# Kernel optimization log

Measured on AMD Instinct MI355X. Metric: run time of the kernel, lower is better.

The kernel has to match this reference:

```python
import jax, jax.numpy as jnp
import numpy as np

B, T_SRC, T_TGT = 32, 64, 64
V_KO, V_EN, E, H = 32000, 32000, 512, 512  # decoder hidden = 2H


def _lstm_step(x, h, c, Wih, Whh, b):
    # PyTorch gate order: i, f, g, o
    g = x @ Wih.T + h @ Whh.T + b
    i, f, gg, o = jnp.split(g, 4, axis=-1)
    c = jax.nn.sigmoid(f) * c + jax.nn.sigmoid(i) * jnp.tanh(gg)
    h = jax.nn.sigmoid(o) * jnp.tanh(c)
    return h, c


def _run_lstm(emb, Wih, Whh, b, hdim):
    # emb: [T, B, E] -> outputs [T, B, hdim], last (h, c)
    nb = emb.shape[1]
    init = (jnp.zeros((nb, hdim), emb.dtype), jnp.zeros((nb, hdim), emb.dtype))
    def step(carry, x):
        h, c = _lstm_step(x, carry[0], carry[1], Wih, Whh, b)
        return (h, c), h
    (h, c), outs = jax.lax.scan(step, init, emb)
    return outs, h, c


def setup_inputs() -> dict:
    key = jax.random.key(0)
    ks = jax.random.split(key, 16)
    s = 0.05
    d = {
        "inp": jax.random.randint(ks[0], (B, T_SRC), 0, V_KO),
        "tar": jax.random.randint(ks[1], (B, T_TGT), 0, V_EN),
        "enc_emb": jax.random.normal(ks[2], (V_KO, E)) * s,
        "dec_emb": jax.random.normal(ks[3], (V_EN, E)) * s,
        # BiLSTM encoder (forward / backward directions)
        "Wih_f": jax.random.normal(ks[4], (4 * H, E)) * s,
        "Whh_f": jax.random.normal(ks[5], (4 * H, H)) * s,
        "b_f": jnp.zeros((4 * H,)),
        "Wih_b": jax.random.normal(ks[6], (4 * H, E)) * s,
        "Whh_b": jax.random.normal(ks[7], (4 * H, H)) * s,
        "b_b": jnp.zeros((4 * H,)),
        # Concat (Bahdanau) attention: W [2H, 4H], v [2H]
        "Wa": jax.random.normal(ks[8], (2 * H, 4 * H)) * s,
        "va": jax.random.normal(ks[9], (2 * H,)) * s,
        # Decoder LSTMCell: input E + 2H, hidden 2H
        "Wih_d": jax.random.normal(ks[10], (8 * H, E + 2 * H)) * s,
        "Whh_d": jax.random.normal(ks[11], (8 * H, 2 * H)) * s,
        "b_d": jnp.zeros((8 * H,)),
        # Output projection
        "Wout": jax.random.normal(ks[12], (V_EN, 2 * H)) * s,
        "bout": jnp.zeros((V_EN,)),
    }
    return d


def reference(inp, tar, enc_emb, dec_emb, Wih_f, Whh_f, b_f, Wih_b, Whh_b, b_b,
              Wa, va, Wih_d, Whh_d, b_d, Wout, bout):
    # ---- Encoder: BiLSTM over source ----
    emb = enc_emb[inp].transpose(1, 0, 2)  # [T_src, B, E]
    out_f, hf, cf = _run_lstm(emb, Wih_f, Whh_f, b_f, H)
    out_b, hb, cb = _run_lstm(emb[::-1], Wih_b, Whh_b, b_b, H)
    enc_out = jnp.concatenate([out_f, out_b[::-1]], axis=-1)  # [T_src, B, 2H]
    h = jnp.concatenate([hf, hb], axis=-1)  # [B, 2H]
    c = jnp.concatenate([cf, cb], axis=-1)

    # ---- Decoder: teacher forcing with concat attention ----
    dec_e = dec_emb[tar].transpose(1, 0, 2)  # [T_tgt, B, E]
    Tsrc = enc_out.shape[0]

    def step(carry, x):
        h, c = carry
        hq = jnp.broadcast_to(h[None], (Tsrc,) + h.shape)         # [T_src, B, 2H]
        energy = jnp.tanh(jnp.concatenate([hq, enc_out], -1) @ Wa.T)  # [T_src, B, 2H]
        score = energy @ va                                        # [T_src, B]
        alpha = jax.nn.softmax(score, axis=0)
        cvec = jnp.einsum('tb,tbh->bh', alpha, enc_out)            # [B, 2H]
        h2, c2 = _lstm_step(jnp.concatenate([x, cvec], -1), h, c, Wih_d, Whh_d, b_d)
        return (h2, c2), h2

    _, hs = jax.lax.scan(step, (h, c), dec_e)  # [T_tgt, B, 2H]
    hs = hs.transpose(1, 0, 2)                 # [B, T_tgt, 2H]
    logits = jax.nn.relu(hs @ Wout.T + bout)   # [B, T_tgt, V_en]
    return jax.nn.log_softmax(logits, axis=2)
```

## Files before the change

kernel.cpp:

```cpp
#include <hip/hip_runtime.h>
#include <stdint.h>
#include <stddef.h>


using u16 = unsigned short;
using u32 = unsigned int;
using short8 = __attribute__((ext_vector_type(8))) short;
using f32x4  = __attribute__((ext_vector_type(4))) float;

#define DEVI __device__ __forceinline__

DEVI float bf2f(u16 u){ union{u32 i; float f;} v; v.i = ((u32)u)<<16; return v.f; }
DEVI u16 f2bf(float f){ union{float f; u32 i;} v; v.f = f;
  u32 r = (v.i + 0x7fffu + ((v.i>>16)&1u)) >> 16; return (u16)r; }
DEVI float sigf(float x){ x = fminf(fmaxf(x,-30.f),30.f); return 1.f/(1.f+__expf(-x)); }
DEVI float tanh_f(float x){ float ax = fminf(fabsf(x),15.f);
  float e = __expf(2.f*ax); float t = (e-1.f)/(e+1.f); return x<0.f? -t : t; }

DEVI f32x4 mfma16(short8 a, short8 b, f32x4 c){
  return __builtin_amdgcn_mfma_f32_16x16x32_bf16(a,b,c,0,0,0);
}
DEVI short8 ld8(const u16* p){ return *(const short8*)p; }

DEVI void storeC(float* C, size_t i, float v){ C[i]=v; }
DEVI void storeC(u16*   C, size_t i, float v){ C[i]=f2bf(v); }

__global__ void gather_emb(const int* __restrict__ inp, const int* __restrict__ tar,
                           const u16* __restrict__ enc_emb, const u16* __restrict__ dec_emb,
                           u16* __restrict__ emb_src, u16* __restrict__ dec_e)
{
  int row = blockIdx.x;
  int t = row >> 5, b = row & 31;
  int d = blockIdx.y;
  int idx = (d ? tar : inp)[b*64 + t];
  const uint4* src = (const uint4*)((d ? dec_emb : enc_emb) + (size_t)idx*512);
  uint4*       dst = (uint4*)((d ? dec_e : emb_src) + (size_t)row*512);
  dst[threadIdx.x] = src[threadIdx.x];
}

__global__ void zero_u16k(u16* __restrict__ p, int n){
  int i = blockIdx.x*blockDim.x + threadIdx.x; if(i<n) p[i]=0;
}

template<int BIAS, int RELU, typename OutT>
__global__ void __launch_bounds__(256) gemm_bt(
  const u16* __restrict__ A, int lda,
  const u16* __restrict__ W, int ldw,
  const u16* __restrict__ bias,
  OutT* __restrict__ C, int ldc, int K)
{
  int lane = threadIdx.x & 63, w = threadIdx.x >> 6;
  int wm = w >> 1, wn = w & 1;
  int bm = blockIdx.y*64 + wm*32, bn = blockIdx.x*64 + wn*32;
  int q = lane >> 4, col = lane & 15;
  const u16* a0p = A + (size_t)(bm + col)*lda + q*8;
  const u16* a1p = a0p + (size_t)16*lda;
  const u16* b0p = W + (size_t)(bn + col)*ldw + q*8;
  const u16* b1p = b0p + (size_t)16*ldw;
  f32x4 z = {0.f,0.f,0.f,0.f};
  f32x4 acc[2][2] = {{z,z},{z,z}};
  for(int k=0;k<K;k+=32){
    short8 a0 = ld8(a0p + k);
    short8 a1 = ld8(a1p + k);
    short8 b0 = ld8(b0p + k);
    short8 b1 = ld8(b1p + k);
    acc[0][0] = mfma16(a0,b0,acc[0][0]);
    acc[0][1] = mfma16(a0,b1,acc[0][1]);
    acc[1][0] = mfma16(a1,b0,acc[1][0]);
    acc[1][1] = mfma16(a1,b1,acc[1][1]);
  }
  #pragma unroll
  for(int fm=0; fm<2; fm++){
    #pragma unroll
    for(int fn=0; fn<2; fn++){
      int colg = bn + fn*16 + col;
      float bia = BIAS ? bf2f(bias[colg]) : 0.f;
      #pragma unroll
      for(int r=0;r<4;r++){
        int rowg = bm + fm*16 + q*4 + r;
        float x = acc[fm][fn][r] + bia;
        if(RELU) x = fmaxf(x, 0.f);
        storeC(C, (size_t)rowg*ldc + colg, x);
      }
    }
  }
}

__global__ void __launch_bounds__(256) gemm_m32(
  const u16* __restrict__ A, int lda,
  const u16* __restrict__ W, int ldw,
  float* __restrict__ C, int ldc, int K)
{
  int lane = threadIdx.x & 63, w = threadIdx.x >> 6;
  int bn = blockIdx.x*64 + w*16;
  int q = lane>>4, col = lane&15;
  const u16* ap = A + (size_t)col*lda + q*8;
  const u16* wp = W + (size_t)(bn+col)*ldw + q*8;
  f32x4 z = {0.f,0.f,0.f,0.f};
  f32x4 acc0=z, acc1=z;
  for(int k=0;k<K;k+=32){
    short8 a0 = ld8(ap + k);
    short8 a1 = ld8(ap + (size_t)16*lda + k);
    short8 b  = ld8(wp + k);
    acc0 = mfma16(a0,b,acc0); acc1 = mfma16(a1,b,acc1);
  }
  #pragma unroll
  for(int r=0;r<4;r++){
    C[(size_t)(q*4 + r)*ldc + bn + col]      = acc0[r];
    C[(size_t)(16 + q*4 + r)*ldc + bn + col] = acc1[r];
  }
}

__global__ void __launch_bounds__(256) enc_cell(
  const u16* __restrict__ Whh_f, const u16* __restrict__ Whh_b,
  const u16* __restrict__ Xf, const u16* __restrict__ Xb,
  const u16* __restrict__ hin, u16* __restrict__ hout,
  float* __restrict__ c_enc,
  u16* __restrict__ enc_out,
  u16* __restrict__ A0h, float* __restrict__ c_buf,
  int s)
{
  int tid = threadIdx.x, lane = tid&63, w = tid>>6;
  int dir = blockIdx.y, j0 = blockIdx.x*16;
  int q = lane>>4, col = lane&15;
  const u16* W  = dir ? Whh_b : Whh_f;
  const u16* Xp = dir ? Xb : Xf;
  int t = dir ? 63 - s : s;
  int n = w*512 + j0 + col;
  const u16* wp = W + (size_t)n*512 + q*8;
  const u16* ap = hin + (size_t)(dir*32 + col)*512 + q*8;
  f32x4 z = {0.f,0.f,0.f,0.f};
  f32x4 acc0=z, acc1=z;
  for(int kk=0; kk<512; kk+=32){
    short8 a0 = ld8(ap + kk);
    short8 a1 = ld8(ap + 16*512 + kk);
    short8 b  = ld8(wp + kk);
    acc0 = mfma16(a0,b,acc0); acc1 = mfma16(a1,b,acc1);
  }
  __shared__ float gl[4][32][16];
  #pragma unroll
  for(int r=0;r<4;r++){
    gl[w][q*4+r][col]      = acc0[r];
    gl[w][16+q*4+r][col]   = acc1[r];
  }
  __syncthreads();
  for(int i = tid; i < 512; i += 256){
    int b_ = i>>4, jl = i&15, j = j0 + jl;
    size_t xrow = (size_t)(t*32 + b_)*2048;
    float gi = gl[0][b_][jl] + bf2f(Xp[xrow + j]);
    float gf = gl[1][b_][jl] + bf2f(Xp[xrow + 512 + j]);
    float gg = gl[2][b_][jl] + bf2f(Xp[xrow + 1024 + j]);
    float go = gl[3][b_][jl] + bf2f(Xp[xrow + 1536 + j]);
    int ci = (dir*32 + b_)*512 + j;
    float c = s ? c_enc[ci] : 0.f;
    float cn = sigf(gf)*c + sigf(gi)*tanh_f(gg);
    float hn = sigf(go)*tanh_f(cn);
    c_enc[ci] = cn;
    u16 hb = f2bf(hn);
    hout[(size_t)(dir*32 + b_)*512 + j] = hb;
    enc_out[(size_t)(t*32 + b_)*1024 + dir*512 + j] = hb;
    if(s==63){
      A0h[b_*2048 + 1024 + dir*512 + j] = hb;
      c_buf[b_*1024 + dir*512 + j] = cn;
    }
  }
}

__global__ void __launch_bounds__(1024) att_kernel(
  const float* __restrict__ hWa1,
  const u16* __restrict__ encWa2,
  const u16* __restrict__ va,
  const u16* __restrict__ enc_out,
  u16* __restrict__ Acur)
{
  int b = blockIdx.x, tid = threadIdx.x;
  __shared__ float e_s[1024], va_s[1024], sc_s[64], al_s[64];
  e_s[tid]  = hWa1[b*1024 + tid];
  va_s[tid] = bf2f(va[tid]);
  __syncthreads();
  int t16 = tid >> 4, l16 = tid & 15;
  const u16* erow = encWa2 + (size_t)(t16*32 + b)*1024;
  float pacc = 0.f;
  for(int j = l16; j < 1024; j += 16)
    pacc += tanh_f(e_s[j] + bf2f(erow[j])) * va_s[j];
  #pragma unroll
  for(int off=8; off; off>>=1) pacc += __shfl_down(pacc, off, 16);
  if(l16==0) sc_s[t16] = pacc;
  __syncthreads();
  if(tid < 64){
    float sv = sc_s[tid];
    float m = sv;
    #pragma unroll
    for(int off=32; off; off>>=1) m = fmaxf(m, __shfl_xor(m, off, 64));
    float e = __expf(sv - m);
    float ssum = e;
    #pragma unroll
    for(int off=32; off; off>>=1) ssum += __shfl_xor(ssum, off, 64);
    al_s[tid] = e / ssum;
  }
  __syncthreads();
  float cv = 0.f;
  for(int tt=0; tt<64; tt++)
    cv += al_s[tt] * bf2f(enc_out[(size_t)(tt*32 + b)*1024 + tid]);
  Acur[b*2048 + tid] = f2bf(cv);
}

__global__ void __launch_bounds__(512) dec_cell(
  const u16* __restrict__ A,
  const u16* __restrict__ Wih_d,
  const u16* __restrict__ Whh_d,
  const u16* __restrict__ Xd,
  float* __restrict__ c_buf,
  u16* __restrict__ Anext,
  u16* __restrict__ hs,
  int t)
{
  int tid = threadIdx.x, lane = tid & 63, w = tid >> 6;
  int g = w & 3, kh = w >> 2;
  int j0 = blockIdx.x * 16;
  int q = lane >> 4, col = lane & 15;
  int n = g*1024 + j0 + col;
  const u16* wp = kh ? (Whh_d + (size_t)n*1024 + q*8)
                     : (Wih_d + (size_t)n*1536 + 512 + q*8);
  const u16* ap = A + (size_t)col*2048 + kh*1024 + q*8;
  f32x4 z = {0.f,0.f,0.f,0.f};
  f32x4 acc0=z, acc1=z;
  for(int kk=0; kk<1024; kk+=32){
    short8 a0 = ld8(ap + kk);
    short8 a1 = ld8(ap + 16*2048 + kk);
    short8 b  = ld8(wp + kk);
    acc0 = mfma16(a0,b,acc0); acc1 = mfma16(a1,b,acc1);
  }
  __shared__ float gp[2][4][32][16];
  #pragma unroll
  for(int r=0;r<4;r++){
    gp[kh][g][q*4+r][col]    = acc0[r];
    gp[kh][g][16+q*4+r][col] = acc1[r];
  }
  __syncthreads();
  {
    int b_ = tid >> 4, jl = tid & 15, j = j0 + jl;
    size_t xrow = (size_t)(t*32 + b_)*4096;
    float gi = gp[0][0][b_][jl] + gp[1][0][b_][jl] + bf2f(Xd[xrow + j]);
    float gf = gp[0][1][b_][jl] + gp[1][1][b_][jl] + bf2f(Xd[xrow + 1024 + j]);
    float gg = gp[0][2][b_][jl] + gp[1][2][b_][jl] + bf2f(Xd[xrow + 2048 + j]);
    float go = gp[0][3][b_][jl] + gp[1][3][b_][jl] + bf2f(Xd[xrow + 3072 + j]);
    float c = c_buf[b_*1024 + j];
    float cn = sigf(gf)*c + sigf(gi)*tanh_f(gg);
    float hn = sigf(go)*tanh_f(cn);
    c_buf[b_*1024 + j] = cn;
    u16 hb = f2bf(hn);
    Anext[b_*2048 + 1024 + j] = hb;
    hs[(size_t)(b_*64 + t)*1024 + j] = hb;
  }
}

__global__ void __launch_bounds__(256) log_softmax_rows(float* __restrict__ out)
{
  int r = blockIdx.x, tid = threadIdx.x;
  float* row = out + (size_t)r*32000;
  const float4* row4 = (const float4*)row;
  __shared__ float rbuf[16];
  float m = -1e30f;
  for(int c = tid; c < 8000; c += 256){
    float4 u = row4[c];
    m = fmaxf(m, fmaxf(fmaxf(u.x,u.y), fmaxf(u.z,u.w)));
  }
  #pragma unroll
  for(int off=32; off; off>>=1) m = fmaxf(m, __shfl_down(m, off, 64));
  if((tid&63)==0) rbuf[tid>>6] = m;
  __syncthreads();
  if(tid==0) rbuf[8] = fmaxf(fmaxf(rbuf[0],rbuf[1]), fmaxf(rbuf[2],rbuf[3]));
  __syncthreads();
  float M = rbuf[8];
  float s = 0.f;
  for(int c = tid; c < 8000; c += 256){
    float4 u = row4[c];
    s += __expf(u.x-M) + __expf(u.y-M) + __expf(u.z-M) + __expf(u.w-M);
  }
  #pragma unroll
  for(int off=32; off; off>>=1) s += __shfl_down(s, off, 64);
  if((tid&63)==0) rbuf[4 + (tid>>6)] = s;
  __syncthreads();
  if(tid==0) rbuf[9] = M + logf(rbuf[4]+rbuf[5]+rbuf[6]+rbuf[7]);
  __syncthreads();
  float L = rbuf[9];
  float4* row4w = (float4*)row;
  for(int c = tid; c < 8000; c += 256){
    float4 u = row4[c];
    u.x -= L; u.y -= L; u.z -= L; u.w -= L;
    row4w[c] = u;
  }
}

extern "C" void kernel_launch(void* const* d_in, const int* in_sizes, int n_in,
                              void* d_out, int out_size, void* d_ws, size_t ws_size,
                              hipStream_t stream)
{
  (void)in_sizes; (void)n_in; (void)out_size; (void)ws_size;
  const int* inp     = (const int*)d_in[0];
  const int* tar     = (const int*)d_in[1];
  const u16* enc_emb = (const u16*)d_in[2];
  const u16* dec_emb = (const u16*)d_in[3];
  const u16* Wih_f   = (const u16*)d_in[4];
  const u16* Whh_f   = (const u16*)d_in[5];
  const u16* b_f     = (const u16*)d_in[6];
  const u16* Wih_b   = (const u16*)d_in[7];
  const u16* Whh_b   = (const u16*)d_in[8];
  const u16* b_b     = (const u16*)d_in[9];
  const u16* Wa      = (const u16*)d_in[10];
  const u16* va      = (const u16*)d_in[11];
  const u16* Wih_d   = (const u16*)d_in[12];
  const u16* Whh_d   = (const u16*)d_in[13];
  const u16* b_d     = (const u16*)d_in[14];
  const u16* Wout    = (const u16*)d_in[15];
  const u16* bout    = (const u16*)d_in[16];

  char* p = (char*)d_ws;
  auto carve = [&](size_t bytes)->char*{
    char* r = p; p += (bytes + 255) & ~(size_t)255; return r; };
  u16*   emb_src = (u16*)  carve(2048ull*512*2);
  u16*   dec_e   = (u16*)  carve(2048ull*512*2);
  u16*   Xf      = (u16*)  carve(2048ull*2048*2);
  u16*   Xb      = (u16*)  carve(2048ull*2048*2);
  u16*   Xd      = (u16*)  carve(2048ull*4096*2);
  u16*   enc_out = (u16*)  carve(2048ull*1024*2);
  u16*   encWa2  = (u16*)  carve(2048ull*1024*2);
  u16*   h_enc   = (u16*)  carve(2ull*2*32*512*2);
  float* c_enc   = (float*)carve(2ull*32*512*4);
  u16*   A_buf   = (u16*)  carve(2ull*32*2048*2);
  float* c_buf   = (float*)carve(32ull*1024*4);
  float* hWa1    = (float*)carve(32ull*1024*4);
  u16*   hs      = (u16*)  carve(2048ull*1024*2);

  gather_emb<<<dim3(2048,2),64,0,stream>>>(inp,tar,enc_emb,dec_emb,emb_src,dec_e);
  zero_u16k<<<128,256,0,stream>>>(h_enc, 2*32*512);

  gemm_bt<1,0,u16><<<dim3(32,32),256,0,stream>>>(emb_src,512, Wih_f,512,  b_f, Xf,2048, 512);
  gemm_bt<1,0,u16><<<dim3(32,32),256,0,stream>>>(emb_src,512, Wih_b,512,  b_b, Xb,2048, 512);
  gemm_bt<1,0,u16><<<dim3(64,32),256,0,stream>>>(dec_e,  512, Wih_d,1536, b_d, Xd,4096, 512);

  for(int s=0;s<64;s++){
    u16* hin  = h_enc + (s&1)*2*32*512;
    u16* hout = h_enc + ((s+1)&1)*2*32*512;
    enc_cell<<<dim3(32,2),256,0,stream>>>(Whh_f,Whh_b, Xf,Xb, hin,hout,
                                          c_enc, enc_out, A_buf, c_buf, s);
  }

  gemm_bt<0,0,u16><<<dim3(16,32),256,0,stream>>>(enc_out,1024, Wa+1024,2048,
                                                 nullptr, encWa2,1024, 1024);

  for(int t=0;t<64;t++){
    u16* Acur  = A_buf + (t&1)*32*2048;
    u16* Anext = A_buf + ((t+1)&1)*32*2048;
    gemm_m32<<<16,256,0,stream>>>(Acur+1024, 2048, Wa, 2048, hWa1, 1024, 1024);
    att_kernel<<<32,1024,0,stream>>>(hWa1, encWa2, va, enc_out, Acur);
    dec_cell<<<64,512,0,stream>>>(Acur, Wih_d, Whh_d, Xd, c_buf, Anext, hs, t);
  }

  gemm_bt<1,1,float><<<dim3(500,32),256,0,stream>>>(hs,1024, Wout,1024, bout,
                                                    (float*)d_out,32000, 1024);
  log_softmax_rows<<<2048,256,0,stream>>>((float*)d_out);
}
```

Measured before the change: 6.162 ms.

## Replace per-step encoder and decoder launches with persistent kernels using grid barriers

```diff
diff --git a/kernel.cpp b/kernel.cpp
--- a/kernel.cpp
+++ b/kernel.cpp
@@ -24,6 +24,28 @@
 
 DEVI void storeC(float* C, size_t i, float v){ C[i]=v; }
 DEVI void storeC(u16*   C, size_t i, float v){ C[i]=f2bf(v); }
+
+DEVI void gbar(unsigned* bar, unsigned nb){
+  __syncthreads();
+  if(threadIdx.x==0){
+    __threadfence();
+    unsigned g = __hip_atomic_load(bar+1, __ATOMIC_RELAXED, __HIP_MEMORY_SCOPE_AGENT);
+    unsigned a = __hip_atomic_fetch_add(bar, 1u, __ATOMIC_ACQ_REL, __HIP_MEMORY_SCOPE_AGENT);
+    if(a == nb-1u){
+      __hip_atomic_store(bar, 0u, __ATOMIC_RELAXED, __HIP_MEMORY_SCOPE_AGENT);
+      __hip_atomic_fetch_add(bar+1, 1u, __ATOMIC_ACQ_REL, __HIP_MEMORY_SCOPE_AGENT);
+    } else {
+      while(__hip_atomic_load(bar+1, __ATOMIC_ACQUIRE, __HIP_MEMORY_SCOPE_AGENT) == g)
+        __builtin_amdgcn_s_sleep(2);
+    }
+    __threadfence();
+  }
+  __syncthreads();
+}
+
+__global__ void zero_bar(unsigned* __restrict__ bar){
+  if(threadIdx.x < 2) bar[threadIdx.x] = 0u;
+}
 
 __global__ void gather_emb(const int* __restrict__ inp, const int* __restrict__ tar,
                            const u16* __restrict__ enc_emb, const u16* __restrict__ dec_emb,
@@ -36,10 +58,6 @@
   const uint4* src = (const uint4*)((d ? dec_emb : enc_emb) + (size_t)idx*512);
   uint4*       dst = (uint4*)((d ? dec_e : emb_src) + (size_t)row*512);
   dst[threadIdx.x] = src[threadIdx.x];
-}
-
-__global__ void zero_u16k(u16* __restrict__ p, int n){
-  int i = blockIdx.x*blockDim.x + threadIdx.x; if(i<n) p[i]=0;
 }
 
 template<int BIAS, int RELU, typename OutT>
@@ -86,172 +104,212 @@
   }
 }
 
-__global__ void __launch_bounds__(256) gemm_m32(
-  const u16* __restrict__ A, int lda,
-  const u16* __restrict__ W, int ldw,
-  float* __restrict__ C, int ldc, int K)
-{
-  int lane = threadIdx.x & 63, w = threadIdx.x >> 6;
-  int bn = blockIdx.x*64 + w*16;
-  int q = lane>>4, col = lane&15;
-  const u16* ap = A + (size_t)col*lda + q*8;
-  const u16* wp = W + (size_t)(bn+col)*ldw + q*8;
-  f32x4 z = {0.f,0.f,0.f,0.f};
-  f32x4 acc0=z, acc1=z;
-  for(int k=0;k<K;k+=32){
-    short8 a0 = ld8(ap + k);
-    short8 a1 = ld8(ap + (size_t)16*lda + k);
-    short8 b  = ld8(wp + k);
-    acc0 = mfma16(a0,b,acc0); acc1 = mfma16(a1,b,acc1);
-  }
-  #pragma unroll
-  for(int r=0;r<4;r++){
-    C[(size_t)(q*4 + r)*ldc + bn + col]      = acc0[r];
-    C[(size_t)(16 + q*4 + r)*ldc + bn + col] = acc1[r];
-  }
-}
-
-__global__ void __launch_bounds__(256) enc_cell(
+#define ENC_NB 64u
+__global__ void __launch_bounds__(256) enc_persist(
   const u16* __restrict__ Whh_f, const u16* __restrict__ Whh_b,
   const u16* __restrict__ Xf, const u16* __restrict__ Xb,
-  const u16* __restrict__ hin, u16* __restrict__ hout,
+  u16* h_enc,
   float* __restrict__ c_enc,
   u16* __restrict__ enc_out,
   u16* __restrict__ A0h, float* __restrict__ c_buf,
-  int s)
+  unsigned* __restrict__ bar)
 {
   int tid = threadIdx.x, lane = tid&63, w = tid>>6;
-  int dir = blockIdx.y, j0 = blockIdx.x*16;
+  int blk = blockIdx.x;
+  int dir = blk >> 5, j0 = (blk & 31)*16;
   int q = lane>>4, col = lane&15;
   const u16* W  = dir ? Whh_b : Whh_f;
   const u16* Xp = dir ? Xb : Xf;
-  int t = dir ? 63 - s : s;
   int n = w*512 + j0 + col;
   const u16* wp = W + (size_t)n*512 + q*8;
-  const u16* ap = hin + (size_t)(dir*32 + col)*512 + q*8;
-  f32x4 z = {0.f,0.f,0.f,0.f};
-  f32x4 acc0=z, acc1=z;
-  for(int kk=0; kk<512; kk+=32){
-    short8 a0 = ld8(ap + kk);
-    short8 a1 = ld8(ap + 16*512 + kk);
-    short8 b  = ld8(wp + kk);
-    acc0 = mfma16(a0,b,acc0); acc1 = mfma16(a1,b,acc1);
-  }
   __shared__ float gl[4][32][16];
-  #pragma unroll
-  for(int r=0;r<4;r++){
-    gl[w][q*4+r][col]      = acc0[r];
-    gl[w][16+q*4+r][col]   = acc1[r];
-  }
-  __syncthreads();
-  for(int i = tid; i < 512; i += 256){
-    int b_ = i>>4, jl = i&15, j = j0 + jl;
-    size_t xrow = (size_t)(t*32 + b_)*2048;
-    float gi = gl[0][b_][jl] + bf2f(Xp[xrow + j]);
-    float gf = gl[1][b_][jl] + bf2f(Xp[xrow + 512 + j]);
-    float gg = gl[2][b_][jl] + bf2f(Xp[xrow + 1024 + j]);
-    float go = gl[3][b_][jl] + bf2f(Xp[xrow + 1536 + j]);
-    int ci = (dir*32 + b_)*512 + j;
-    float c = s ? c_enc[ci] : 0.f;
-    float cn = sigf(gf)*c + sigf(gi)*tanh_f(gg);
-    float hn = sigf(go)*tanh_f(cn);
-    c_enc[ci] = cn;
-    u16 hb = f2bf(hn);
-    hout[(size_t)(dir*32 + b_)*512 + j] = hb;
-    enc_out[(size_t)(t*32 + b_)*1024 + dir*512 + j] = hb;
-    if(s==63){
-      A0h[b_*2048 + 1024 + dir*512 + j] = hb;
-      c_buf[b_*1024 + dir*512 + j] = cn;
-    }
-  }
-}
-
-__global__ void __launch_bounds__(1024) att_kernel(
-  const float* __restrict__ hWa1,
-  const u16* __restrict__ encWa2,
+
+  for(int s=0;s<64;s++){
+    int t = dir ? 63 - s : s;
+    f32x4 z = {0.f,0.f,0.f,0.f};
+    f32x4 acc0=z, acc1=z;
+    if(s){
+      const u16* hin = h_enc + (size_t)(s&1)*2*32*512;
+      const u16* ap = hin + (size_t)(dir*32 + col)*512 + q*8;
+      for(int kk=0; kk<512; kk+=32){
+        short8 a0 = ld8(ap + kk);
+        short8 a1 = ld8(ap + 16*512 + kk);
+        short8 b  = ld8(wp + kk);
+        acc0 = mfma16(a0,b,acc0); acc1 = mfma16(a1,b,acc1);
+      }
+    }
+    #pragma unroll
+    for(int r=0;r<4;r++){
+      gl[w][q*4+r][col]    = acc0[r];
+      gl[w][16+q*4+r][col] = acc1[r];
+    }
+    __syncthreads();
+    u16* hout = h_enc + (size_t)((s+1)&1)*2*32*512;
+    for(int i = tid; i < 512; i += 256){
+      int b_ = i>>4, jl = i&15, j = j0 + jl;
+      size_t xrow = (size_t)(t*32 + b_)*2048;
+      float gi = gl[0][b_][jl] + bf2f(Xp[xrow + j]);
+      float gf = gl[1][b_][jl] + bf2f(Xp[xrow + 512 + j]);
+      float gg = gl[2][b_][jl] + bf2f(Xp[xrow + 1024 + j]);
+      float go = gl[3][b_][jl] + bf2f(Xp[xrow + 1536 + j]);
+      int ci = (dir*32 + b_)*512 + j;
+      float c = s ? c_enc[ci] : 0.f;
+      float cn = sigf(gf)*c + sigf(gi)*tanh_f(gg);
+      float hn = sigf(go)*tanh_f(cn);
+      c_enc[ci] = cn;
+      u16 hb = f2bf(hn);
+      hout[(size_t)(dir*32 + b_)*512 + j] = hb;
+      enc_out[(size_t)(t*32 + b_)*1024 + dir*512 + j] = hb;
+      if(s==63){
+        A0h[b_*2048 + 1024 + dir*512 + j] = hb;
+        c_buf[b_*1024 + dir*512 + j] = cn;
+      }
+    }
+    gbar(bar, ENC_NB);
+  }
+}
+
+#define DEC_NB 80u
+__global__ void __launch_bounds__(512,2) dec_persist(
+  u16* A_buf,
+  const u16* __restrict__ Wa,
   const u16* __restrict__ va,
-  const u16* __restrict__ enc_out,
-  u16* __restrict__ Acur)
-{
-  int b = blockIdx.x, tid = threadIdx.x;
-  __shared__ float e_s[1024], va_s[1024], sc_s[64], al_s[64];
-  e_s[tid]  = hWa1[b*1024 + tid];
-  va_s[tid] = bf2f(va[tid]);
-  __syncthreads();
-  int t16 = tid >> 4, l16 = tid & 15;
-  const u16* erow = encWa2 + (size_t)(t16*32 + b)*1024;
-  float pacc = 0.f;
-  for(int j = l16; j < 1024; j += 16)
-    pacc += tanh_f(e_s[j] + bf2f(erow[j])) * va_s[j];
-  #pragma unroll
-  for(int off=8; off; off>>=1) pacc += __shfl_down(pacc, off, 16);
-  if(l16==0) sc_s[t16] = pacc;
-  __syncthreads();
-  if(tid < 64){
-    float sv = sc_s[tid];
-    float m = sv;
-    #pragma unroll
-    for(int off=32; off; off>>=1) m = fmaxf(m, __shfl_xor(m, off, 64));
-    float e = __expf(sv - m);
-    float ssum = e;
-    #pragma unroll
-    for(int off=32; off; off>>=1) ssum += __shfl_xor(ssum, off, 64);
-    al_s[tid] = e / ssum;
-  }
-  __syncthreads();
-  float cv = 0.f;
-  for(int tt=0; tt<64; tt++)
-    cv += al_s[tt] * bf2f(enc_out[(size_t)(tt*32 + b)*1024 + tid]);
-  Acur[b*2048 + tid] = f2bf(cv);
-}
-
-__global__ void __launch_bounds__(512) dec_cell(
-  const u16* __restrict__ A,
   const u16* __restrict__ Wih_d,
   const u16* __restrict__ Whh_d,
   const u16* __restrict__ Xd,
+  const u16* __restrict__ encWa2,
+  const u16* __restrict__ enc_out,
+  float* __restrict__ hWa1,
   float* __restrict__ c_buf,
-  u16* __restrict__ Anext,
   u16* __restrict__ hs,
-  int t)
+  unsigned* __restrict__ bar)
 {
   int tid = threadIdx.x, lane = tid & 63, w = tid >> 6;
+  int blk = blockIdx.x;
+  int q = lane >> 4, col = lane & 15;
   int g = w & 3, kh = w >> 2;
-  int j0 = blockIdx.x * 16;
-  int q = lane >> 4, col = lane & 15;
-  int n = g*1024 + j0 + col;
-  const u16* wp = kh ? (Whh_d + (size_t)n*1024 + q*8)
-                     : (Wih_d + (size_t)n*1536 + 512 + q*8);
-  const u16* ap = A + (size_t)col*2048 + kh*1024 + q*8;
-  f32x4 z = {0.f,0.f,0.f,0.f};
-  f32x4 acc0=z, acc1=z;
-  for(int kk=0; kk<1024; kk+=32){
-    short8 a0 = ld8(ap + kk);
-    short8 a1 = ld8(ap + 16*2048 + kk);
-    short8 b  = ld8(wp + kk);
-    acc0 = mfma16(a0,b,acc0); acc1 = mfma16(a1,b,acc1);
-  }
+
   __shared__ float gp[2][4][32][16];
-  #pragma unroll
-  for(int r=0;r<4;r++){
-    gp[kh][g][q*4+r][col]    = acc0[r];
-    gp[kh][g][16+q*4+r][col] = acc1[r];
-  }
-  __syncthreads();
-  {
-    int b_ = tid >> 4, jl = tid & 15, j = j0 + jl;
-    size_t xrow = (size_t)(t*32 + b_)*4096;
-    float gi = gp[0][0][b_][jl] + gp[1][0][b_][jl] + bf2f(Xd[xrow + j]);
-    float gf = gp[0][1][b_][jl] + gp[1][1][b_][jl] + bf2f(Xd[xrow + 1024 + j]);
-    float gg = gp[0][2][b_][jl] + gp[1][2][b_][jl] + bf2f(Xd[xrow + 2048 + j]);
-    float go = gp[0][3][b_][jl] + gp[1][3][b_][jl] + bf2f(Xd[xrow + 3072 + j]);
-    float c = c_buf[b_*1024 + j];
-    float cn = sigf(gf)*c + sigf(gi)*tanh_f(gg);
-    float hn = sigf(go)*tanh_f(cn);
-    c_buf[b_*1024 + j] = cn;
-    u16 hb = f2bf(hn);
-    Anext[b_*2048 + 1024 + j] = hb;
-    hs[(size_t)(b_*64 + t)*1024 + j] = hb;
+  __shared__ float e_s[1024], va_s[1024], sc_s[64], al_s[64];
+  if(blk < 32){ va_s[tid] = bf2f(va[tid]); va_s[tid+512] = bf2f(va[tid+512]); }
+
+  int dblk = blk & 63;
+  int n = g*1024 + dblk*16 + col;
+  const u16* wp1 = Whh_d + (size_t)n*1024 + kh*512 + q*8;
+  const u16* wp3 = Wih_d + (size_t)n*1536 + 512 + kh*512 + q*8;
+  int mb = (blk >= 64) ? (blk - 64) : 0;
+  int nm = mb*64 + g*16 + col;
+  const u16* wpm = Wa + (size_t)nm*2048 + kh*512 + q*8;
+
+  for(int t=0;t<64;t++){
+    u16* Acur  = A_buf + (size_t)(t&1)*32*2048;
+    u16* Anext = A_buf + (size_t)((t+1)&1)*32*2048;
+    f32x4 z = {0.f,0.f,0.f,0.f};
+    f32x4 acc0=z, acc1=z;
+
+    if(blk < 64){
+      const u16* ap = Acur + (size_t)col*2048 + 1024 + kh*512 + q*8;
+      for(int kk=0; kk<512; kk+=32){
+        short8 a0 = ld8(ap + kk);
+        short8 a1 = ld8(ap + 16*2048 + kk);
+        short8 b  = ld8(wp1 + kk);
+        acc0 = mfma16(a0,b,acc0); acc1 = mfma16(a1,b,acc1);
+      }
+    } else {
+      const u16* ap = Acur + (size_t)col*2048 + 1024 + kh*512 + q*8;
+      f32x4 m0=z, m1=z;
+      for(int kk=0; kk<512; kk+=32){
+        short8 a0 = ld8(ap + kk);
+        short8 a1 = ld8(ap + 16*2048 + kk);
+        short8 b  = ld8(wpm + kk);
+        m0 = mfma16(a0,b,m0); m1 = mfma16(a1,b,m1);
+      }
+      #pragma unroll
+      for(int r=0;r<4;r++){
+        gp[kh][g][q*4+r][col]    = m0[r];
+        gp[kh][g][16+q*4+r][col] = m1[r];
+      }
+      __syncthreads();
+      for(int i=tid; i<2048; i+=512){
+        int b_ = i>>6, cc = i&63;
+        hWa1[b_*1024 + mb*64 + cc] = gp[0][cc>>4][b_][cc&15] + gp[1][cc>>4][b_][cc&15];
+      }
+    }
+    gbar(bar, DEC_NB);
+
+    if(blk < 32){
+      int b = blk;
+      e_s[tid]     = hWa1[b*1024 + tid];
+      e_s[tid+512] = hWa1[b*1024 + 512 + tid];
+      __syncthreads();
+      int grp = tid>>4, l16 = tid&15;
+      #pragma unroll
+      for(int half=0; half<2; half++){
+        int ts = grp + half*32;
+        const u16* erow = encWa2 + ((size_t)ts*32 + b)*1024;
+        float pacc = 0.f;
+        for(int j = l16; j < 1024; j += 16)
+          pacc += tanh_f(e_s[j] + bf2f(erow[j])) * va_s[j];
+        #pragma unroll
+        for(int off=8; off; off>>=1) pacc += __shfl_down(pacc, off, 16);
+        if(l16==0) sc_s[ts] = pacc;
+      }
+      __syncthreads();
+      if(tid < 64){
+        float sv = sc_s[tid];
+        float m = sv;
+        #pragma unroll
+        for(int off=32; off; off>>=1) m = fmaxf(m, __shfl_xor(m, off, 64));
+        float e = __expf(sv - m);
+        float ssum = e;
+        #pragma unroll
+        for(int off=32; off; off>>=1) ssum += __shfl_xor(ssum, off, 64);
+        al_s[tid] = e / ssum;
+      }
+      __syncthreads();
+      float cv0 = 0.f, cv1 = 0.f;
+      for(int tt=0; tt<64; tt++){
+        float a = al_s[tt];
+        const u16* er = enc_out + ((size_t)tt*32 + b)*1024;
+        cv0 += a * bf2f(er[tid]);
+        cv1 += a * bf2f(er[512 + tid]);
+      }
+      Acur[b*2048 + tid]       = f2bf(cv0);
+      Acur[b*2048 + 512 + tid] = f2bf(cv1);
+    }
+    gbar(bar, DEC_NB);
+
+    if(blk < 64){
+      const u16* ap = Acur + (size_t)col*2048 + kh*512 + q*8;
+      for(int kk=0; kk<512; kk+=32){
+        short8 a0 = ld8(ap + kk);
+        short8 a1 = ld8(ap + 16*2048 + kk);
+        short8 b  = ld8(wp3 + kk);
+        acc0 = mfma16(a0,b,acc0); acc1 = mfma16(a1,b,acc1);
+      }
+      #pragma unroll
+      for(int r=0;r<4;r++){
+        gp[kh][g][q*4+r][col]    = acc0[r];
+        gp[kh][g][16+q*4+r][col] = acc1[r];
+      }
+      __syncthreads();
+      {
+        int b_ = tid >> 4, jl = tid & 15, j = dblk*16 + jl;
+        size_t xrow = (size_t)(t*32 + b_)*4096;
+        float gi = gp[0][0][b_][jl] + gp[1][0][b_][jl] + bf2f(Xd[xrow + j]);
+        float gf = gp[0][1][b_][jl] + gp[1][1][b_][jl] + bf2f(Xd[xrow + 1024 + j]);
+        float gg = gp[0][2][b_][jl] + gp[1][2][b_][jl] + bf2f(Xd[xrow + 2048 + j]);
+        float go = gp[0][3][b_][jl] + gp[1][3][b_][jl] + bf2f(Xd[xrow + 3072 + j]);
+        float c = c_buf[b_*1024 + j];
+        float cn = sigf(gf)*c + sigf(gi)*tanh_f(gg);
+        float hn = sigf(go)*tanh_f(cn);
+        c_buf[b_*1024 + j] = cn;
+        u16 hb = f2bf(hn);
+        Anext[b_*2048 + 1024 + j] = hb;
+        hs[(size_t)(b_*64 + t)*1024 + j] = hb;
+      }
+    }
+    gbar(bar, DEC_NB);
   }
 }
 
@@ -332,31 +390,23 @@
   float* c_buf   = (float*)carve(32ull*1024*4);
   float* hWa1    = (float*)carve(32ull*1024*4);
   u16*   hs      = (u16*)  carve(2048ull*1024*2);
-
+  unsigned* bar  = (unsigned*)carve(256);
+
+  zero_bar<<<1,64,0,stream>>>(bar);
   gather_emb<<<dim3(2048,2),64,0,stream>>>(inp,tar,enc_emb,dec_emb,emb_src,dec_e);
-  zero_u16k<<<128,256,0,stream>>>(h_enc, 2*32*512);
 
   gemm_bt<1,0,u16><<<dim3(32,32),256,0,stream>>>(emb_src,512, Wih_f,512,  b_f, Xf,2048, 512);
   gemm_bt<1,0,u16><<<dim3(32,32),256,0,stream>>>(emb_src,512, Wih_b,512,  b_b, Xb,2048, 512);
   gemm_bt<1,0,u16><<<dim3(64,32),256,0,stream>>>(dec_e,  512, Wih_d,1536, b_d, Xd,4096, 512);
 
-  for(int s=0;s<64;s++){
-    u16* hin  = h_enc + (s&1)*2*32*512;
-    u16* hout = h_enc + ((s+1)&1)*2*32*512;
-    enc_cell<<<dim3(32,2),256,0,stream>>>(Whh_f,Whh_b, Xf,Xb, hin,hout,
-                                          c_enc, enc_out, A_buf, c_buf, s);
-  }
+  enc_persist<<<64,256,0,stream>>>(Whh_f,Whh_b, Xf,Xb, h_enc, c_enc,
+                                   enc_out, A_buf, c_buf, bar);
 
   gemm_bt<0,0,u16><<<dim3(16,32),256,0,stream>>>(enc_out,1024, Wa+1024,2048,
                                                  nullptr, encWa2,1024, 1024);
 
-  for(int t=0;t<64;t++){
-    u16* Acur  = A_buf + (t&1)*32*2048;
-    u16* Anext = A_buf + ((t+1)&1)*32*2048;
-    gemm_m32<<<16,256,0,stream>>>(Acur+1024, 2048, Wa, 2048, hWa1, 1024, 1024);
-    att_kernel<<<32,1024,0,stream>>>(hWa1, encWa2, va, enc_out, Acur);
-    dec_cell<<<64,512,0,stream>>>(Acur, Wih_d, Whh_d, Xd, c_buf, Anext, hs, t);
-  }
+  dec_persist<<<80,512,0,stream>>>(A_buf, Wa, va, Wih_d, Whh_d, Xd,
+                                   encWa2, enc_out, hWa1, c_buf, hs, bar);
 
   gemm_bt<1,1,float><<<dim3(500,32),256,0,stream>>>(hs,1024, Wout,1024, bout,
                                                     (float*)d_out,32000, 1024);
```

Result: slower. 11.54 ms (+87.2%).
